# Kernel optimization log

Measured on AMD Instinct MI355X. Metric: run time of the kernel, lower is better.

Reference implementation:

```python
import jax, jax.numpy as jnp
import numpy as np

B, L, D = 4, 4096, 1024


def setup_inputs() -> dict:
    key = jax.random.key(0)
    ks = jax.random.split(key, 10)
    x = jax.random.normal(ks[0], (B, L, D), dtype=jnp.float32)
    time_decay = jax.random.normal(ks[1], (D,), dtype=jnp.float32) * 0.1 - 5.0
    time_first = jax.random.normal(ks[2], (D,), dtype=jnp.float32) * 0.01
    time_mix_k = jnp.ones((D,), jnp.float32) * 0.5
    time_mix_v = jnp.ones((D,), jnp.float32) * 0.5
    time_mix_r = jnp.ones((D,), jnp.float32) * 0.5
    s = 1.0 / np.sqrt(D)
    Wk = jax.random.normal(ks[3], (D, D), dtype=jnp.float32) * s
    Wv = jax.random.normal(ks[4], (D, D), dtype=jnp.float32) * s
    Wr = jax.random.normal(ks[5], (D, D), dtype=jnp.float32) * s
    Wo = jax.random.normal(ks[6], (D, D), dtype=jnp.float32) * s
    return {"x": x, "time_decay": time_decay, "time_first": time_first,
            "time_mix_k": time_mix_k, "time_mix_v": time_mix_v, "time_mix_r": time_mix_r,
            "Wk": Wk, "Wv": Wv, "Wr": Wr, "Wo": Wo}


def _wkv_scan(k, v, w, u):
    # k, v: [B, L, D]; w, u: [D]. Sequential linear recurrence over L.
    decay = jnp.exp(w)  # per-channel decay factor e^{w}, w = -exp(time_decay) < 0
    Bb, Ll, Dd = k.shape

    def step(carry, kv_t):
        a, b = carry  # [B, D] numerator / denominator states
        k_t, v_t = kv_t
        ek_u = jnp.exp(u + k_t)
        wkv = (a + ek_u * v_t) / jnp.maximum(b + ek_u, 1e-6)
        ek = jnp.exp(k_t)
        return (decay * a + ek * v_t, decay * b + ek), wkv

    init = (jnp.zeros((Bb, Dd), k.dtype), jnp.zeros((Bb, Dd), k.dtype))
    _, out = jax.lax.scan(step, init, (jnp.swapaxes(k, 0, 1), jnp.swapaxes(v, 0, 1)))
    return jnp.swapaxes(out, 0, 1)  # [B, L, D]


def reference(x, time_decay, time_first, time_mix_k, time_mix_v, time_mix_r, Wk, Wv, Wr, Wo):
    Ll = x.shape[1]
    # token shift: x_prev[t] = x[t-1], zeros at t=0
    x_prev = jnp.pad(x, ((0, 0), (1, 0), (0, 0)))[:, :Ll]
    xk = x * time_mix_k + x_prev * (1.0 - time_mix_k)
    xv = x * time_mix_v + x_prev * (1.0 - time_mix_v)
    xr = x * time_mix_r + x_prev * (1.0 - time_mix_r)
    k = jnp.einsum('bld,ed->ble', xk, Wk)
    v = jnp.einsum('bld,ed->ble', xv, Wv)
    r = jax.nn.sigmoid(jnp.einsum('bld,ed->ble', xr, Wr))
    w = -jnp.exp(time_decay)
    wkv = _wkv_scan(k, v, w, time_first)
    return jnp.einsum('bld,ed->ble', r * wkv, Wo)
```

## Files before the change

### kernel.cpp

```cpp
#include <hip/hip_runtime.h>
#include <cstdint>
#include <cstddef>

typedef __bf16 bf16;
typedef __bf16 bf16x4 __attribute__((ext_vector_type(4)));
typedef __bf16 bf16x8 __attribute__((ext_vector_type(8)));
typedef float floatx4 __attribute__((ext_vector_type(4)));
typedef float floatx8 __attribute__((ext_vector_type(8)));
typedef unsigned int u32;

constexpr int Bb = 4, Ll = 4096, Dd = 1024;
constexpr int M  = Bb * Ll;
constexpr int NC = 64, CT = 64;

typedef const __attribute__((address_space(1))) u32 glb_u32;
typedef __attribute__((address_space(3))) u32 lds_u32;
__device__ __forceinline__ void gld16(const bf16* g, bf16* l) {
  __builtin_amdgcn_global_load_lds((glb_u32*)g, (lds_u32*)l, 16, 0, 0);
}
__device__ __forceinline__ void bar() {
  __builtin_amdgcn_s_barrier();
  asm volatile("" ::: "memory");
}

__global__ __launch_bounds__(256) void convw(
    const float* __restrict__ W, bf16* __restrict__ Wb)
{
  size_t base = ((size_t)blockIdx.x * 256 + threadIdx.x) * 8;
  floatx8 w = *(const floatx8*)(W + base);
  bf16x8 o;
  #pragma unroll
  for (int j = 0; j < 8; ++j) o[j] = (bf16)w[j];
  *(bf16x8*)(Wb + base) = o;
}

__global__ __launch_bounds__(256) void convw3(
    const float* __restrict__ Wa, const float* __restrict__ Wbp, const float* __restrict__ Wc,
    bf16* __restrict__ oa, bf16* __restrict__ ob, bf16* __restrict__ oc)
{
  const float* s = blockIdx.y == 0 ? Wa : (blockIdx.y == 1 ? Wbp : Wc);
  bf16*        d = blockIdx.y == 0 ? oa : (blockIdx.y == 1 ? ob  : oc);
  size_t base = ((size_t)blockIdx.x * 256 + threadIdx.x) * 8;
  floatx8 w = *(const floatx8*)(s + base);
  bf16x8 o;
  #pragma unroll
  for (int j = 0; j < 8; ++j) o[j] = (bf16)w[j];
  *(bf16x8*)(d + base) = o;
}

__global__ __launch_bounds__(256) void prep3(
    const float* __restrict__ x, const float* __restrict__ ma, const float* __restrict__ mb,
    const float* __restrict__ mc,
    bf16* __restrict__ oa, bf16* __restrict__ ob, bf16* __restrict__ oc)
{
  size_t base = ((size_t)blockIdx.x * 256 + threadIdx.x) * 8;
  int d = (int)(base & (size_t)(Dd - 1));
  int l = (int)((base / Dd) & (size_t)(Ll - 1));
  floatx8 xc = *(const floatx8*)(x + base);
  floatx8 xp = l ? *(const floatx8*)(x + base - Dd) : (floatx8)(0.0f);
  floatx8 a = *(const floatx8*)(ma + d);
  floatx8 b = *(const floatx8*)(mb + d);
  floatx8 c = *(const floatx8*)(mc + d);
  bf16x8 ra, rb, rc;
  #pragma unroll
  for (int j = 0; j < 8; ++j) {
    ra[j] = (bf16)(xc[j] * a[j] + xp[j] * (1.0f - a[j]));
    rb[j] = (bf16)(xc[j] * b[j] + xp[j] * (1.0f - b[j]));
    rc[j] = (bf16)(xc[j] * c[j] + xp[j] * (1.0f - c[j]));
  }
  *(bf16x8*)(oa + base) = ra;
  *(bf16x8*)(ob + base) = rb;
  *(bf16x8*)(oc + base) = rc;
}

template <int ACT>
__global__ __launch_bounds__(512, 4) void gemmP(
    const bf16* __restrict__ A, const bf16* __restrict__ W, void* __restrict__ Cout)
{
  __shared__ __align__(16) bf16 sm[36864];
  const int tid  = threadIdx.x;
  const int lane = tid & 63;
  const int w    = tid >> 6;
  const int wm   = (w >> 2) * 64;
  const int wn   = (w & 3) * 64;
  const int fr   = lane & 15;
  const int cu   = lane >> 4;
  const int soff = ((cu ^ ((fr >> 1) & 3)) << 3);

  const int flat = (int)(blockIdx.y * 4 + blockIdx.x);
  const int nid  = (flat & 7) * 64 + (flat >> 3);
  const int m0   = (nid >> 2) * 128, n0 = (nid & 3) * 256;

  const int rA  = tid >> 2;
  const int cA  = (((tid & 3) ^ ((rA >> 1) & 3)) << 3);
  const int uB1 = tid + 512;
  const int rB0 = tid >> 2, cB0 = cA;
  const int rB1 = uB1 >> 2, cB1 = (((uB1 & 3) ^ ((rB1 >> 1) & 3)) << 3);
  const bf16* gA  = A + (size_t)(m0 + rA)  * Dd + cA;
  const bf16* gB0 = W + (size_t)(n0 + rB0) * Dd + cB0;
  const bf16* gB1 = W + (size_t)(n0 + rB1) * Dd + cB1;

  auto stage = [&](int slot, int t) {
    const size_t kt = (size_t)(t > 31 ? 31 : t) * 32;
    bf16* s = sm + slot * 12288;
    gld16(gA  + kt, s + (size_t)tid * 8);
    gld16(gB0 + kt, s + 4096 + (size_t)tid * 8);
    gld16(gB1 + kt, s + 4096 + (size_t)uB1 * 8);
  };

  floatx4 acc[4][4];
  #pragma unroll
  for (int i = 0; i < 4; ++i)
    #pragma unroll
    for (int j = 0; j < 4; ++j)
      acc[i][j] = (floatx4)(0.0f);

  stage(0, 0);
  stage(1, 1);

  bf16x8 a[4], b[4];
  int scur = 0;
  for (int t = 0; t < 32; ++t) {
    asm volatile("s_waitcnt vmcnt(3)" ::: "memory");
    bar();
    int sstg = scur + 2; if (sstg >= 3) sstg -= 3;
    stage(sstg, t + 2);

    const bf16* sA = sm + scur * 12288;
    const bf16* sB = sA + 4096;
    #pragma unroll
    for (int i = 0; i < 4; ++i)
      a[i] = *(const bf16x8*)(sA + (wm + fr + i * 16) * 32 + soff);
    #pragma unroll
    for (int j = 0; j < 4; ++j)
      b[j] = *(const bf16x8*)(sB + (wn + fr + j * 16) * 32 + soff);

    __builtin_amdgcn_s_setprio(1);
    #pragma unroll
    for (int i = 0; i < 4; ++i)
      #pragma unroll
      for (int j = 0; j < 4; ++j)
        acc[i][j] = __builtin_amdgcn_mfma_f32_16x16x32_bf16(a[i], b[j], acc[i][j], 0, 0, 0);
    __builtin_amdgcn_s_setprio(0);

    scur = (scur + 1 == 3) ? 0 : scur + 1;
  }
  asm volatile("s_waitcnt vmcnt(0)" ::: "memory");

  #pragma unroll
  for (int mi = 0; mi < 4; ++mi) {
    int rbase = m0 + wm + mi * 16 + (lane >> 4) * 4;
    #pragma unroll
    for (int j = 0; j < 4; ++j) {
      int col = n0 + wn + j * 16 + (lane & 15);
      #pragma unroll
      for (int r = 0; r < 4; ++r) {
        float v = acc[mi][j][r];
        size_t off = (size_t)(rbase + r) * Dd + col;
        if (ACT == 0)      ((float*)Cout)[off] = v;
        else if (ACT == 1) ((bf16*)Cout)[off]  = (bf16)(1.0f / (1.0f + __expf(-v)));
        else               ((bf16*)Cout)[off]  = (bf16)v;
      }
    }
  }
}

__global__ __launch_bounds__(256) void scan_partial(
    const bf16* __restrict__ k, const bf16* __restrict__ v,
    const float* __restrict__ td, float* __restrict__ Pa, float* __restrict__ Pb)
{
  const int pair = blockIdx.x;
  const int b = pair >> 6, c = pair & (NC - 1);
  const int d0 = threadIdx.x * 4;
  floatx4 tdv = *(const floatx4*)(td + d0);
  float decay[4], pa[4], pb[4];
  #pragma unroll
  for (int j = 0; j < 4; ++j) {
    decay[j] = __expf(-__expf(tdv[j]));
    pa[j] = 0.0f; pb[j] = 0.0f;
  }
  size_t base = ((size_t)(b * Ll + c * CT)) * Dd + d0;
  #pragma unroll 4
  for (int t = 0; t < CT; ++t) {
    size_t idx = base + (size_t)t * Dd;
    bf16x4 kk = *(const bf16x4*)(k + idx);
    bf16x4 vv = *(const bf16x4*)(v + idx);
    #pragma unroll
    for (int j = 0; j < 4; ++j) {
      float ek = __expf((float)kk[j]);
      pa[j] = decay[j] * pa[j] + ek * (float)vv[j];
      pb[j] = decay[j] * pb[j] + ek;
    }
  }
  size_t o = (size_t)pair * Dd + d0;
  floatx4 outa, outb;
  #pragma unroll
  for (int j = 0; j < 4; ++j) { outa[j] = pa[j]; outb[j] = pb[j]; }
  *(floatx4*)(Pa + o) = outa;
  *(floatx4*)(Pb + o) = outb;
}

__global__ __launch_bounds__(256) void scan_combine(
    const float* __restrict__ td, const float* __restrict__ Pa, const float* __restrict__ Pb,
    float* __restrict__ A0, float* __restrict__ B0)
{
  int d = blockIdx.x * 256 + threadIdx.x;
  int b = blockIdx.y;
  float dT = __expf(-__expf(td[d]) * (float)CT);
  float a = 0.0f, bb = 0.0f;
  for (int c = 0; c < NC; ++c) {
    size_t o = ((size_t)(b * NC + c)) * Dd + d;
    A0[o] = a; B0[o] = bb;
    a  = dT * a  + Pa[o];
    bb = dT * bb + Pb[o];
  }
}

__global__ __launch_bounds__(256) void scan_final(
    const bf16* __restrict__ k, bf16* __restrict__ vy, const bf16* __restrict__ r,
    const float* __restrict__ td, const float* __restrict__ tf,
    const float* __restrict__ A0, const float* __restrict__ B0)
{
  const int pair = blockIdx.x;
  const int b = pair >> 6, c = pair & (NC - 1);
  const int d0 = threadIdx.x * 4;
  floatx4 tdv = *(const floatx4*)(td + d0);
  floatx4 tfv = *(const floatx4*)(tf + d0);
  size_t o = (size_t)pair * Dd + d0;
  floatx4 av = *(const floatx4*)(A0 + o);
  floatx4 bv = *(const floatx4*)(B0 + o);
  float decay[4], u[4], a[4], bb[4];
  #pragma unroll
  for (int j = 0; j < 4; ++j) {
    decay[j] = __expf(-__expf(tdv[j]));
    u[j] = tfv[j]; a[j] = av[j]; bb[j] = bv[j];
  }
  size_t base = ((size_t)(b * Ll + c * CT)) * Dd + d0;
  #pragma unroll 2
  for (int t = 0; t < CT; ++t) {
    size_t idx = base + (size_t)t * Dd;
    bf16x4 kk = *(const bf16x4*)(k + idx);
    bf16x4 vv = *(const bf16x4*)(vy + idx);
    bf16x4 rr4 = *(const bf16x4*)(r + idx);
    bf16x4 y;
    #pragma unroll
    for (int j = 0; j < 4; ++j) {
      float kkj = (float)kk[j];
      float vvj = (float)vv[j];
      float eku = __expf(u[j] + kkj);
      float wkv = (a[j] + eku * vvj) / fmaxf(bb[j] + eku, 1e-6f);
      y[j] = (bf16)((float)rr4[j] * wkv);
      float ek = __expf(kkj);
      a[j]  = decay[j] * a[j]  + ek * vvj;
      bb[j] = decay[j] * bb[j] + ek;
    }
    *(bf16x4*)(vy + idx) = y;
  }
}

extern "C" void kernel_launch(void* const* d_in, const int* in_sizes, int n_in,
                              void* d_out, int out_size, void* d_ws, size_t ws_size,
                              hipStream_t stream)
{
  const float* x  = (const float*)d_in[0];
  const float* td = (const float*)d_in[1];
  const float* tf = (const float*)d_in[2];
  const float* mk = (const float*)d_in[3];
  const float* mv = (const float*)d_in[4];
  const float* mr = (const float*)d_in[5];
  const float* Wk = (const float*)d_in[6];
  const float* Wv = (const float*)d_in[7];
  const float* Wr = (const float*)d_in[8];
  const float* Wo = (const float*)d_in[9];
  float* out = (float*)d_out;

  char* ws = (char*)d_ws;
  const size_t S2 = (size_t)M * Dd * sizeof(bf16);
  const size_t SP = (size_t)Bb * NC * Dd;
  bf16* buf1 = (bf16*)(ws);
  bf16* buf2 = (bf16*)(ws + S2);
  bf16* buf3 = (bf16*)(ws + 2 * S2);
  float* Pa = (float*)(ws + 3 * S2);
  float* Pb = Pa + SP;
  float* A0 = Pb + SP;
  float* B0 = A0 + SP;

  char* ob  = (char*)d_out;
  bf16* rr  = (bf16*)d_out;
  bf16* Wkb = (bf16*)(ob + ((size_t)32 << 20));
  bf16* Wvb = (bf16*)(ob + ((size_t)34 << 20));
  bf16* Wrb = (bf16*)(ob + ((size_t)36 << 20));
  bf16* Wob = (bf16*)Pa;

  dim3 gp((unsigned)((size_t)M * Dd / (256 * 8)));
  dim3 gw((unsigned)((size_t)Dd * Dd / (256 * 8)));
  dim3 gg(Dd / 256, M / 128);

  convw3<<<dim3(gw.x, 3), 256, 0, stream>>>(Wk, Wv, Wr, Wkb, Wvb, Wrb);

  prep3<<<gp, 256, 0, stream>>>(x, mk, mv, mr, buf1, buf2, buf3);

  gemmP<1><<<gg, 512, 0, stream>>>(buf3, Wrb, rr);
  gemmP<2><<<gg, 512, 0, stream>>>(buf1, Wkb, buf3);
  gemmP<2><<<gg, 512, 0, stream>>>(buf2, Wvb, buf1);

  scan_partial<<<dim3(Bb * NC), 256, 0, stream>>>(buf3, buf1, td, Pa, Pb);
  scan_combine<<<dim3(Dd / 256, Bb), 256, 0, stream>>>(td, Pa, Pb, A0, B0);
  convw<<<gw, 256, 0, stream>>>(Wo, Wob);
  scan_final  <<<dim3(Bb * NC), 256, 0, stream>>>(buf3, buf1, rr, td, tf, A0, B0);

  gemmP<0><<<gg, 512, 0, stream>>>(buf1, Wob, out);
}
```

Baseline: 348.3 us.

## Enlarge GEMM tiles to 256x256 with 4-stage split-phase pipeline

Replaces the 128x256 GEMM tile with a 256x256 tile per 512-thread block, so each wave computes a 128x64 output. Operand loads now go through a 4-slot LDS ring with prefetch depth 3, and the A and B stages are interleaved between two half-MFMA phases separated by extra barriers. The aim is to cut global and LDS traffic per FLOP and hide memory latency better. In exchange, occupancy drops (launch bounds 2, 128KB LDS), the accumulator register footprint doubles, and each iteration adds barriers.

```diff
diff --git a/kernel.cpp b/kernel.cpp
--- a/kernel.cpp
+++ b/kernel.cpp
@@ -74,81 +74,100 @@
 }
 
 template <int ACT>
-__global__ __launch_bounds__(512, 4) void gemmP(
+__global__ __launch_bounds__(512, 2) void gemmQ(
     const bf16* __restrict__ A, const bf16* __restrict__ W, void* __restrict__ Cout)
 {
-  __shared__ __align__(16) bf16 sm[36864];
+  __shared__ __align__(16) bf16 sm[65536];
   const int tid  = threadIdx.x;
   const int lane = tid & 63;
   const int w    = tid >> 6;
-  const int wm   = (w >> 2) * 64;
+  const int wm   = (w >> 2) * 128;
   const int wn   = (w & 3) * 64;
   const int fr   = lane & 15;
   const int cu   = lane >> 4;
   const int soff = ((cu ^ ((fr >> 1) & 3)) << 3);
 
   const int flat = (int)(blockIdx.y * 4 + blockIdx.x);
-  const int nid  = (flat & 7) * 64 + (flat >> 3);
-  const int m0   = (nid >> 2) * 128, n0 = (nid & 3) * 256;
-
-  const int rA  = tid >> 2;
-  const int cA  = (((tid & 3) ^ ((rA >> 1) & 3)) << 3);
-  const int uB1 = tid + 512;
-  const int rB0 = tid >> 2, cB0 = cA;
-  const int rB1 = uB1 >> 2, cB1 = (((uB1 & 3) ^ ((rB1 >> 1) & 3)) << 3);
-  const bf16* gA  = A + (size_t)(m0 + rA)  * Dd + cA;
-  const bf16* gB0 = W + (size_t)(n0 + rB0) * Dd + cB0;
-  const bf16* gB1 = W + (size_t)(n0 + rB1) * Dd + cB1;
-
-  auto stage = [&](int slot, int t) {
+  const int q    = flat >> 3, r8 = flat & 7;
+  const int mp   = r8 + 8 * (q >> 2);
+  const int nb   = q & 3;
+  const int m0   = mp * 256, n0 = nb * 256;
+
+  const int u0 = tid, u1 = tid + 512;
+  const int r0 = u0 >> 2, c0 = (((u0 & 3) ^ ((r0 >> 1) & 3)) << 3);
+  const int r1 = u1 >> 2, c1 = (((u1 & 3) ^ ((r1 >> 1) & 3)) << 3);
+  const bf16* gA0 = A + (size_t)(m0 + r0) * Dd + c0;
+  const bf16* gA1 = A + (size_t)(m0 + r1) * Dd + c1;
+  const bf16* gB0 = W + (size_t)(n0 + r0) * Dd + c0;
+  const bf16* gB1 = W + (size_t)(n0 + r1) * Dd + c1;
+
+  auto stageA = [&](int slot, int t) {
     const size_t kt = (size_t)(t > 31 ? 31 : t) * 32;
-    bf16* s = sm + slot * 12288;
-    gld16(gA  + kt, s + (size_t)tid * 8);
-    gld16(gB0 + kt, s + 4096 + (size_t)tid * 8);
-    gld16(gB1 + kt, s + 4096 + (size_t)uB1 * 8);
+    bf16* s = sm + slot * 16384;
+    gld16(gA0 + kt, s + (size_t)u0 * 8);
+    gld16(gA1 + kt, s + (size_t)u1 * 8);
   };
-
-  floatx4 acc[4][4];
-  #pragma unroll
-  for (int i = 0; i < 4; ++i)
+  auto stageB = [&](int slot, int t) {
+    const size_t kt = (size_t)(t > 31 ? 31 : t) * 32;
+    bf16* s = sm + slot * 16384 + 8192;
+    gld16(gB0 + kt, s + (size_t)u0 * 8);
+    gld16(gB1 + kt, s + (size_t)u1 * 8);
+  };
+
+  floatx4 acc[8][4];
+  #pragma unroll
+  for (int i = 0; i < 8; ++i)
     #pragma unroll
     for (int j = 0; j < 4; ++j)
       acc[i][j] = (floatx4)(0.0f);
 
-  stage(0, 0);
-  stage(1, 1);
-
-  bf16x8 a[4], b[4];
-  int scur = 0;
+  stageA(0, 0); stageB(0, 0);
+  stageA(1, 1); stageB(1, 1);
+  stageA(2, 2); stageB(2, 2);
+
+  bf16x8 a03[4], a47[4], b[4];
   for (int t = 0; t < 32; ++t) {
-    asm volatile("s_waitcnt vmcnt(3)" ::: "memory");
+    const int scur = t & 3;
+    const int sstg = (t + 3) & 3;
+    asm volatile("s_waitcnt vmcnt(8)" ::: "memory");
     bar();
-    int sstg = scur + 2; if (sstg >= 3) sstg -= 3;
-    stage(sstg, t + 2);
-
-    const bf16* sA = sm + scur * 12288;
-    const bf16* sB = sA + 4096;
+    const bf16* sA = sm + scur * 16384;
+    const bf16* sB = sA + 8192;
+
     #pragma unroll
     for (int i = 0; i < 4; ++i)
-      a[i] = *(const bf16x8*)(sA + (wm + fr + i * 16) * 32 + soff);
+      a03[i] = *(const bf16x8*)(sA + (wm + fr + i * 16) * 32 + soff);
     #pragma unroll
     for (int j = 0; j < 4; ++j)
       b[j] = *(const bf16x8*)(sB + (wn + fr + j * 16) * 32 + soff);
-
+    stageA(sstg, t + 3);
+    bar();
     __builtin_amdgcn_s_setprio(1);
     #pragma unroll
     for (int i = 0; i < 4; ++i)
       #pragma unroll
       for (int j = 0; j < 4; ++j)
-        acc[i][j] = __builtin_amdgcn_mfma_f32_16x16x32_bf16(a[i], b[j], acc[i][j], 0, 0, 0);
+        acc[i][j] = __builtin_amdgcn_mfma_f32_16x16x32_bf16(a03[i], b[j], acc[i][j], 0, 0, 0);
     __builtin_amdgcn_s_setprio(0);
-
-    scur = (scur + 1 == 3) ? 0 : scur + 1;
+    bar();
+
+    #pragma unroll
+    for (int i = 0; i < 4; ++i)
+      a47[i] = *(const bf16x8*)(sA + (wm + 64 + fr + i * 16) * 32 + soff);
+    stageB(sstg, t + 3);
+    bar();
+    __builtin_amdgcn_s_setprio(1);
+    #pragma unroll
+    for (int i = 0; i < 4; ++i)
+      #pragma unroll
+      for (int j = 0; j < 4; ++j)
+        acc[i + 4][j] = __builtin_amdgcn_mfma_f32_16x16x32_bf16(a47[i], b[j], acc[i + 4][j], 0, 0, 0);
+    __builtin_amdgcn_s_setprio(0);
   }
   asm volatile("s_waitcnt vmcnt(0)" ::: "memory");
 
   #pragma unroll
-  for (int mi = 0; mi < 4; ++mi) {
+  for (int mi = 0; mi < 8; ++mi) {
     int rbase = m0 + wm + mi * 16 + (lane >> 4) * 4;
     #pragma unroll
     for (int j = 0; j < 4; ++j) {
@@ -294,20 +313,20 @@
 
   dim3 gp((unsigned)((size_t)M * Dd / (256 * 8)));
   dim3 gw((unsigned)((size_t)Dd * Dd / (256 * 8)));
-  dim3 gg(Dd / 256, M / 128);
+  dim3 gg(Dd / 256, M / 256);
 
   convw3<<<dim3(gw.x, 3), 256, 0, stream>>>(Wk, Wv, Wr, Wkb, Wvb, Wrb);
 
   prep3<<<gp, 256, 0, stream>>>(x, mk, mv, mr, buf1, buf2, buf3);
 
-  gemmP<1><<<gg, 512, 0, stream>>>(buf3, Wrb, rr);
-  gemmP<2><<<gg, 512, 0, stream>>>(buf1, Wkb, buf3);
-  gemmP<2><<<gg, 512, 0, stream>>>(buf2, Wvb, buf1);
+  gemmQ<1><<<gg, 512, 0, stream>>>(buf3, Wrb, rr);
+  gemmQ<2><<<gg, 512, 0, stream>>>(buf1, Wkb, buf3);
+  gemmQ<2><<<gg, 512, 0, stream>>>(buf2, Wvb, buf1);
 
   scan_partial<<<dim3(Bb * NC), 256, 0, stream>>>(buf3, buf1, td, Pa, Pb);
   scan_combine<<<dim3(Dd / 256, Bb), 256, 0, stream>>>(td, Pa, Pb, A0, B0);
   convw<<<gw, 256, 0, stream>>>(Wo, Wob);
   scan_final  <<<dim3(Bb * NC), 256, 0, stream>>>(buf3, buf1, rr, td, tf, A0, B0);
 
-  gemmP<0><<<gg, 512, 0, stream>>>(buf1, Wob, out);
-}
+  gemmQ<0><<<gg, 512, 0, stream>>>(buf1, Wob, out);
+}
```

Result: no change. 348.3 us (-0.0%).
